# Performance work log

Hardware: AMD Instinct MI355X
Metric: run time of the kernel (lower is better)

The kernel has to match this reference:

```python
import jax, jax.numpy as jnp
import numpy as np

B, DIM, H, W = 8, 128, 112, 112
WSZ, K = 7, 9
D4 = DIM // 4


def setup_inputs() -> dict:
    key = jax.random.key(0)
    ks = jax.random.split(key, 8)
    w = lambda k, shape: jax.random.normal(k, shape, jnp.float32) * 0.05
    return {
        'x_in': jax.random.normal(ks[0], (B, DIM, H, W), jnp.float32),
        'f_w': w(ks[1], (D4, DIM)), 'f_b': jnp.zeros((D4,), jnp.float32),
        'f_gn_w': jnp.ones((D4,), jnp.float32), 'f_gn_b': jnp.zeros((D4,), jnp.float32),
        'p_w': w(ks[2], (DIM, D4)), 'p_b': jnp.zeros((DIM,), jnp.float32),
        'p_gn_w': jnp.ones((DIM,), jnp.float32), 'p_gn_b': jnp.zeros((DIM,), jnp.float32),
        'r_w': w(ks[3], (DIM, DIM)), 'r_b': jnp.zeros((DIM,), jnp.float32),
        'r_gn_w': jnp.ones((DIM,), jnp.float32), 'r_gn_b': jnp.zeros((DIM,), jnp.float32),
        'e1_w': w(ks[4], (D4, 2 * D4)), 'e1_b': jnp.zeros((D4,), jnp.float32),
        'e2_w': w(ks[5], (1, D4)), 'e2_b': jnp.zeros((1,), jnp.float32),
        'gamma': jnp.ones((1,), jnp.float32), 'beta': jnp.zeros((1,), jnp.float32),
    }


def conv1x1(x, w, b):
    # 1x1 conv == channel matmul. x: (B,C,H,W), w: (O,C)
    return jnp.einsum('bchw,oc->bohw', x, w) + b[None, :, None, None]


def gn1(x, w, b, eps=1e-5):
    # GroupNorm(1, C): normalize over (C,H,W) per sample
    mu = x.mean(axis=(1, 2, 3), keepdims=True)
    var = x.var(axis=(1, 2, 3), keepdims=True)
    xn = (x - mu) * jax.lax.rsqrt(var + eps)
    return xn * w[None, :, None, None] + b[None, :, None, None]


def reference(x_in, f_w, f_b, f_gn_w, f_gn_b, p_w, p_b, p_gn_w, p_gn_b,
              r_w, r_b, r_gn_w, r_gn_b, e1_w, e1_b, e2_w, e2_b, gamma, beta):
    b, c, h, w_ = x_in.shape
    wg = hg = WSZ
    pw, ph = h // wg, w_ // hg  # per-window spatial dims (16,16)

    residual = gn1(conv1x1(x_in, r_w, r_b), r_gn_w, r_gn_b)

    # 'b c (Wg w) (Hg h) -> (b Wg Hg) c w h'
    x = x_in.reshape(b, c, wg, pw, hg, ph).transpose(0, 2, 4, 1, 3, 5)
    x = x.reshape(b * wg * hg, c, pw, ph)

    f = gn1(conv1x1(x, f_w, f_b), f_gn_w, f_gn_b)  # (Bp, D4, pw, ph)
    bp, c4, hp, wp = f.shape
    n = hp * wp

    xf = f.reshape(bp, c4, n).transpose(0, 2, 1)  # (Bp, N, C4) nodes

    gy, gx = jnp.meshgrid(jnp.arange(hp), jnp.arange(wp), indexing='ij')
    grid = jnp.stack([gy, gx], axis=-1).astype(jnp.float32).reshape(n, 2)
    grid = (grid - grid.mean(0)) / (grid.std(0, ddof=1) + 1e-5)  # torch std is unbiased

    xa = jnp.concatenate([xf, jnp.broadcast_to(grid, (bp, n, 2))], axis=-1)
    xn = xa / jnp.maximum(jnp.linalg.norm(xa, axis=-1, keepdims=True), 1e-8)
    sim = jnp.einsum('bnd,bmd->bnm', xn, xn)  # (Bp, N, N) cosine sim
    sim = jnp.where(jnp.eye(n, dtype=bool), -jnp.inf, sim)
    _, topk_idx = jax.lax.top_k(sim, K)  # (Bp, N, K)

    # gather neighbor messages; scatter_add back to row == sum over K (rows are dense)
    msg = jax.vmap(lambda a, i: a[i])(xf, topk_idx)          # (Bp, N, K, C4)
    src = jnp.broadcast_to(xf[:, :, None, :], msg.shape)      # (Bp, N, K, C4)
    ef = jnp.concatenate([src, msg], axis=-1)                 # (Bp, N, K, 2*C4)
    h1 = jax.nn.silu(ef @ e1_w.T + e1_b)
    wgt = jax.nn.sigmoid(h1 @ e2_w.T + e2_b)[..., 0]          # (Bp, N, K)
    out = (msg * wgt[..., None]).sum(axis=2)                  # (Bp, N, C4)

    out = out * gamma + xf * beta
    out = out.reshape(bp, hp, wp, c4).transpose(0, 3, 1, 2)   # (Bp, C4, hp, wp)

    # '(b Wg Hg) c w h -> b c (Wg w) (Hg h)'
    out = out.reshape(b, wg, hg, c4, hp, wp).transpose(0, 3, 1, 4, 2, 5)
    out = out.reshape(b, c4, h, w_)

    out = gn1(conv1x1(out, p_w, p_b), p_gn_w, p_gn_b) + residual
    return out
```

## Files before the change

kernel.cpp:

```cpp
#include <hip/hip_runtime.h>
#include <hip/hip_fp16.h>
#include <math.h>

#define CIN 128
#define C4  32
#define HW  12544
#define KNB 9
#define NWIN 392

__device__ inline double wave_sum(double v) {
#pragma unroll
    for (int off = 32; off; off >>= 1) v += __shfl_down(v, off);
    return v;
}

#define TOP9_INSERT(sv, mi, tv, ti)                                  \
    {                                                                \
        _Pragma("unroll")                                            \
        for (int j = KNB - 1; j >= 1; --j) {                         \
            bool cj  = (sv) > tv[j];                                 \
            bool cjm = (sv) > tv[j - 1];                             \
            tv[j] = cj ? (cjm ? tv[j - 1] : (sv)) : tv[j];           \
            ti[j] = cj ? (cjm ? ti[j - 1] : (mi)) : ti[j];           \
        }                                                            \
        bool c0 = (sv) > tv[0];                                      \
        tv[0] = c0 ? (sv) : tv[0];                                   \
        ti[0] = c0 ? (mi) : ti[0];                                   \
    }

__global__ __launch_bounds__(256) void prep_kernel(
    const float* __restrict__ f_w, const float* __restrict__ r_w,
    const float* __restrict__ p_w,
    double* __restrict__ fw64t, float* __restrict__ rwt_t, float* __restrict__ pwt_t)
{
    const int i = blockIdx.x * 256 + threadIdx.x;
    if (i < 4096)  fw64t[(i & 127) * 32 + (i >> 7)]  = (double)f_w[i];
    if (i < 16384) rwt_t[(i & 127) * 128 + (i >> 7)] = r_w[i];
    if (i < 4096)  pwt_t[(i & 31) * 128 + (i >> 5)]  = p_w[i];
}

__global__ __launch_bounds__(512, 6) void fconv_rstats_kernel(
    const float* __restrict__ x_in,
    const double* __restrict__ fw64t, const float* __restrict__ f_b,
    const float* __restrict__ f_gn_w, const float* __restrict__ f_gn_b,
    const float* __restrict__ rwt_t, const float* __restrict__ r_b,
    float* __restrict__ xfws, double* __restrict__ invnws,
    double* __restrict__ stats)
{
    __shared__ __align__(16) char smem[34944];
    double* vbuf = (double*)smem;
    double* red  = (double*)(smem + 34816);
    const int t = threadIdx.x;

    if (blockIdx.x < NWIN) {
        const int win = blockIdx.x;
        const int b = win / 49, wg = (win / 7) % 7, hg = win % 7;
        const int n = t & 255, s = t >> 8;
        const int py = n >> 4, px = n & 15;
        const int rs = __builtin_amdgcn_readfirstlane(s);

        const float* xb = x_in + (size_t)b * CIN * HW + (size_t)(wg * 16 + py) * 112 + (hg * 16 + px);
        const double* wB = fw64t + 16 * rs;
        double acc[16];
#pragma unroll
        for (int j = 0; j < 16; ++j) acc[j] = 0.0;
#pragma unroll 2
        for (int c = 0; c < CIN; ++c) {
            double xv = (double)xb[(size_t)c * HW];
            const double* wr = wB + c * 32;
#pragma unroll
            for (int j = 0; j < 16; ++j) acc[j] = fma(wr[j], xv, acc[j]);
        }
        double s1 = 0.0, s2 = 0.0;
#pragma unroll
        for (int j = 0; j < 16; ++j) {
            double v = acc[j] + (double)f_b[16 * rs + j];
            acc[j] = v; s1 += v; s2 += v * v;
        }
        s1 = wave_sum(s1); s2 = wave_sum(s2);
        {
            int w = t >> 6;
            if ((t & 63) == 0) { red[w] = s1; red[8 + w] = s2; }
        }
        __syncthreads();
        double rs1 = 0.0, rs2 = 0.0;
#pragma unroll
        for (int w = 0; w < 8; ++w) { rs1 += red[w]; rs2 += red[8 + w]; }
        const double mu   = rs1 * (1.0 / 8192.0);
        const double var  = rs2 * (1.0 / 8192.0) - mu * mu;
        const double rstd = 1.0 / sqrt(var + 1e-5);

        float myv[16];
#pragma unroll
        for (int j = 0; j < 16; ++j) {
            int c = 16 * rs + j;
            myv[j] = (float)((acc[j] - mu) * rstd * (double)f_gn_w[c] + (double)f_gn_b[c]);
        }
        float* xrow = xfws + (size_t)(win * 256 + n) * 36;
#pragma unroll
        for (int q4 = 0; q4 < 4; ++q4) {
            float4 f = { myv[4 * q4], myv[4 * q4 + 1], myv[4 * q4 + 2], myv[4 * q4 + 3] };
            ((float4*)(xrow + 16 * rs))[q4] = f;
        }
        const double ginv = 1.0 / (sqrt(5440.0 / 255.0) + 1e-5);
        const float gyf = (float)(((double)py - 7.5) * ginv);
        const float gxf = (float)(((double)px - 7.5) * ginv);
        if (s == 0) {
            float4 g4 = { gyf, gxf, 0.f, 0.f };
            ((float4*)(xrow + 32))[0] = g4;
        }
        if (s == 1) {
#pragma unroll
            for (int j = 0; j < 16; ++j) vbuf[n * 17 + j] = (double)myv[j];
        }
        __syncthreads();
        if (s == 0) {
            double nrm = 0.0;
#pragma unroll
            for (int j = 0; j < 16; ++j) { double x = (double)myv[j]; nrm += x * x; }
#pragma unroll
            for (int j = 0; j < 16; ++j) { double x = vbuf[n * 17 + j]; nrm += x * x; }
            double xg = (double)gyf; nrm += xg * xg;
            double xh = (double)gxf; nrm += xh * xh;
            invnws[win * 256 + n] = 1.0 / fmax(sqrt(nrm), 1e-8);
        }
    } else {
        const int idx = blockIdx.x - NWIN;
        const int b = idx / 98, rem = idx % 98;
        const int oc = rem / 49, pg = rem % 49;
        const int sh = t >> 8, n = t & 255;
        const int rsh = __builtin_amdgcn_readfirstlane(sh);
        const float* wR = rwt_t + oc * 64 + rsh * 32;
        const float* xb = x_in + (size_t)b * CIN * HW + pg * 256 + n;
        float acc[32];
#pragma unroll
        for (int o = 0; o < 32; ++o) acc[o] = r_b[oc * 64 + rsh * 32 + o];
#pragma unroll 2
        for (int c = 0; c < CIN; ++c) {
            float xv = xb[(size_t)c * HW];
            const float* wr = wR + c * 128;
#pragma unroll
            for (int o = 0; o < 32; ++o) acc[o] = fmaf(wr[o], xv, acc[o]);
        }
        double s1 = 0.0, s2 = 0.0;
#pragma unroll
        for (int o = 0; o < 32; ++o) { double v = (double)acc[o]; s1 += v; s2 += v * v; }
        s1 = wave_sum(s1); s2 = wave_sum(s2);
        {
            int w = t >> 6;
            if ((t & 63) == 0) { red[w] = s1; red[8 + w] = s2; }
        }
        __syncthreads();
        if (t == 0) {
            double a = 0.0, c = 0.0;
#pragma unroll
            for (int w = 0; w < 8; ++w) { a += red[w]; c += red[8 + w]; }
            atomicAdd(&stats[b * 4 + 0], a);
            atomicAdd(&stats[b * 4 + 1], c);
        }
    }
}

__global__ __launch_bounds__(256, 4) void sim_hm_kernel(
    const float* __restrict__ xfws, const double* __restrict__ invnws,
    const float* __restrict__ e1_w,
    float* __restrict__ pval, unsigned char* __restrict__ pidx,
    __half* __restrict__ hmws)
{
    const int bid = blockIdx.x;
    if (bid < 4 * NWIN) {
        const int win = bid >> 2, m0 = (bid & 3) << 6;
        const int n = threadIdx.x;

        double xad[34];
        {
            const float4* own = (const float4*)(xfws + (size_t)(win * 256 + n) * 36);
#pragma unroll
            for (int q = 0; q < 8; ++q) {
                float4 f = own[q];
                xad[q * 4 + 0] = (double)f.x; xad[q * 4 + 1] = (double)f.y;
                xad[q * 4 + 2] = (double)f.z; xad[q * 4 + 3] = (double)f.w;
            }
            float4 g = own[8];
            xad[32] = (double)g.x; xad[33] = (double)g.y;
        }
        const double inv_self = invnws[(size_t)win * 256 + n];
        const float*  xmb  = xfws + (size_t)(win * 256 + m0) * 36;
        const double* invb = invnws + (size_t)win * 256 + m0;

        float tv[KNB]; int ti[KNB];
#pragma unroll
        for (int k = 0; k < KNB; ++k) { tv[k] = -INFINITY; ti[k] = 0; }
#pragma unroll 2
        for (int mm = 0; mm < 64; ++mm) {
            const float* xm = xmb + mm * 36;
            double d0 = 0.0, d1 = 0.0, d2 = 0.0, d3 = 0.0;
#pragma unroll
            for (int q = 0; q < 8; ++q) {
                d0 = fma((double)xm[4 * q + 0], xad[4 * q + 0], d0);
                d1 = fma((double)xm[4 * q + 1], xad[4 * q + 1], d1);
                d2 = fma((double)xm[4 * q + 2], xad[4 * q + 2], d2);
                d3 = fma((double)xm[4 * q + 3], xad[4 * q + 3], d3);
            }
            d0 = fma((double)xm[32], xad[32], d0);
            d1 = fma((double)xm[33], xad[33], d1);
            double d = (d0 + d1) + (d2 + d3);
            float sv = (float)(d * (inv_self * invb[mm]));
            sv = (m0 + mm == n) ? -INFINITY : sv;
            TOP9_INSERT(sv, m0 + mm, tv, ti);
        }
        const size_t base = ((size_t)bid * 256 + n) * 9;
#pragma unroll
        for (int k = 0; k < KNB; ++k) { pval[base + k] = tv[k]; pidx[base + k] = (unsigned char)ti[k]; }
    } else {
        const int idxm = bid - 4 * NWIN;
        const int win = idxm >> 1, half = idxm & 1;
        const int t = threadIdx.x;
        const int n = t & 127;
        const int jh = __builtin_amdgcn_readfirstlane(t >> 7);
        const int gn = half * 128 + n;
        const float4* xr4 = (const float4*)(xfws + (size_t)(win * 256 + gn) * 36);
        float xr[32];
#pragma unroll
        for (int q = 0; q < 8; ++q) {
            float4 f = xr4[q];
            xr[4 * q + 0] = f.x; xr[4 * q + 1] = f.y;
            xr[4 * q + 2] = f.z; xr[4 * q + 3] = f.w;
        }
        __align__(16) __half hv[16];
#pragma unroll
        for (int jj = 0; jj < 16; ++jj) {
            const float* w = e1_w + (16 * jh + jj) * 64 + 32;
            float a = 0.f;
#pragma unroll
            for (int c = 0; c < C4; ++c) a = fmaf(w[c], xr[c], a);
            hv[jj] = __float2half_rn(a);
        }
        float4* dst = (float4*)(hmws + (size_t)(win * 256 + gn) * 32 + 16 * jh);
        dst[0] = ((const float4*)hv)[0];
        dst[1] = ((const float4*)hv)[1];
    }
}

__global__ __launch_bounds__(512, 6) void merge_mlp_kernel(
    const float* __restrict__ xfws, const __half* __restrict__ hmws,
    const float* __restrict__ pval, const unsigned char* __restrict__ pidx,
    const float* __restrict__ e1_w, const float* __restrict__ e1_b,
    const float* __restrict__ e2_w, const float* __restrict__ e2_b,
    const float* __restrict__ gamma, const float* __restrict__ beta,
    float* __restrict__ gnn)
{
    __shared__ __align__(16) char smem[50432];
    __half2* xf2 = (__half2*)smem;
    __half2* hm2 = (__half2*)(smem + 17408);
    __half2* hs2 = (__half2*)(smem + 34816);
    short*   Ti  = (short*)(smem + 43520);
    float*   Wt  = (float*)(smem + 45824);

    const int bid = blockIdx.x;
    const int win = bid >> 1, half = bid & 1;
    const int b = win / 49, wg = (win / 7) % 7, hg = win % 7;
    const int t = threadIdx.x;
    const int nl = t & 127, s = t >> 7;
    const int gn = half * 128 + nl;
    const int rs = __builtin_amdgcn_readfirstlane(s);

    {
        const int r = t >> 1, hh = t & 1;
        const float4* sx = (const float4*)(xfws + (size_t)win * 9216 + r * 36 + hh * 16);
#pragma unroll
        for (int q = 0; q < 4; ++q) {
            float4 f = sx[q];
            xf2[r * 17 + hh * 8 + 2 * q]     = __floats2half2_rn(f.x, f.y);
            xf2[r * 17 + hh * 8 + 2 * q + 1] = __floats2half2_rn(f.z, f.w);
        }
        const uint4* sh = (const uint4*)(hmws + (size_t)win * 8192 + r * 32 + hh * 16);
        uint4 u0 = sh[0], u1 = sh[1];
        unsigned int* d = (unsigned int*)(hm2 + r * 17 + hh * 8);
        d[0] = u0.x; d[1] = u0.y; d[2] = u0.z; d[3] = u0.w;
        d[4] = u1.x; d[5] = u1.y; d[6] = u1.z; d[7] = u1.w;
    }
    __syncthreads();

    {
        float xr[C4];
#pragma unroll
        for (int q = 0; q < 16; ++q) {
            float2 f = __half22float2(xf2[gn * 17 + q]);
            xr[2 * q] = f.x; xr[2 * q + 1] = f.y;
        }
        float hsv[8];
#pragma unroll
        for (int jj = 0; jj < 8; ++jj) {
            const int j = 8 * rs + jj;
            const float* w = e1_w + j * 64;
            float h0 = e1_b[j], h1 = 0.f;
#pragma unroll
            for (int c = 0; c < C4; c += 2) {
                h0 = fmaf(w[c], xr[c], h0);
                h1 = fmaf(w[c + 1], xr[c + 1], h1);
            }
            hsv[jj] = h0 + h1;
        }
#pragma unroll
        for (int u = 0; u < 4; ++u)
            hs2[nl * 17 + 4 * rs + u] = __floats2half2_rn(hsv[2 * u], hsv[2 * u + 1]);
    }
    if (s == 0) {
        float tv[KNB]; int ti[KNB];
#pragma unroll
        for (int k = 0; k < KNB; ++k) { tv[k] = -INFINITY; ti[k] = 0; }
        for (int qd = 0; qd < 4; ++qd) {
            const size_t base = ((size_t)(win * 4 + qd) * 256 + gn) * 9;
#pragma unroll
            for (int k = 0; k < KNB; ++k) {
                float sv = pval[base + k];
                int   mi = (int)pidx[base + k];
                TOP9_INSERT(sv, mi, tv, ti);
            }
        }
#pragma unroll
        for (int k = 0; k < KNB; ++k) Ti[nl * 9 + k] = (short)ti[k];
    }
    __syncthreads();

    {
        float hsr[C4];
#pragma unroll
        for (int q = 0; q < 16; ++q) {
            float2 f = __half22float2(hs2[nl * 17 + q]);
            hsr[2 * q] = f.x; hsr[2 * q + 1] = f.y;
        }
        const float e2b = e2_b[0];
        for (int k = s; k < KNB; k += 4) {
            const int m = (int)Ti[nl * 9 + k];
            float a2 = 0.f;
#pragma unroll
            for (int jp = 0; jp < 16; ++jp) {
                float2 hv = __half22float2(hm2[m * 17 + jp]);
                float h0 = hsr[2 * jp] + hv.x;
                float h1 = hsr[2 * jp + 1] + hv.y;
                float sg0 = 1.f / (1.f + __expf(-h0));
                a2 = fmaf(e2_w[2 * jp], h0 * sg0, a2);
                float sg1 = 1.f / (1.f + __expf(-h1));
                a2 = fmaf(e2_w[2 * jp + 1], h1 * sg1, a2);
            }
            Wt[nl * 9 + k] = 1.f / (1.f + __expf(-(a2 + e2b)));
        }
    }
    __syncthreads();

    {
        short tis[KNB]; float wks[KNB];
#pragma unroll
        for (int k = 0; k < KNB; ++k) { tis[k] = Ti[nl * 9 + k]; wks[k] = Wt[nl * 9 + k]; }
        const float g = gamma[0], be = beta[0];
        const int py = gn >> 4, px = gn & 15;
        float* gp = gnn + (size_t)b * C4 * HW + (size_t)(wg * 16 + py) * 112 + (hg * 16 + px);
        float xo[8];
#pragma unroll
        for (int q = 0; q < 4; ++q) {
            float2 f = __half22float2(xf2[gn * 17 + 4 * rs + q]);
            xo[2 * q] = f.x; xo[2 * q + 1] = f.y;
        }
        float o[8];
#pragma unroll
        for (int cc = 0; cc < 8; ++cc) o[cc] = 0.f;
#pragma unroll
        for (int k = 0; k < KNB; ++k) {
            const int mrow = (int)tis[k] * 17 + 4 * rs;
#pragma unroll
            for (int q = 0; q < 4; ++q) {
                float2 mv = __half22float2(xf2[mrow + q]);
                o[2 * q]     = fmaf(wks[k], mv.x, o[2 * q]);
                o[2 * q + 1] = fmaf(wks[k], mv.y, o[2 * q + 1]);
            }
        }
#pragma unroll
        for (int cc = 0; cc < 8; ++cc) {
            float gl = fmaf(g, o[cc], be * xo[cc]);
            gp[(size_t)(8 * rs + cc) * HW] = gl;
        }
    }
}

__global__ __launch_bounds__(256, 8) void pstats_kernel(
    const float* __restrict__ gnn, const float* __restrict__ p_w,
    const float* __restrict__ p_b, double* __restrict__ stats)
{
    __shared__ double red[16];
    const int idx = blockIdx.x;
    const int b = idx / 98, pg = idx % 98;
    const int t = threadIdx.x;
    const int pix = pg * 128 + (t & 127);
    const int oh = __builtin_amdgcn_readfirstlane(t >> 7);

    const float* gb = gnn + (size_t)b * C4 * HW + pix;
    float g[C4];
#pragma unroll
    for (int c = 0; c < C4; ++c) g[c] = gb[(size_t)c * HW];

    double s1 = 0.0, s2 = 0.0;
    const float* pwb = p_w + (size_t)oh * 64 * C4;
#pragma unroll 4
    for (int o = 0; o < 64; ++o) {
        const float* w = pwb + o * C4;
        float y = p_b[oh * 64 + o];
#pragma unroll
        for (int c = 0; c < C4; ++c) y = fmaf(w[c], g[c], y);
        s1 += (double)y; s2 += (double)y * (double)y;
    }
    s1 = wave_sum(s1); s2 = wave_sum(s2);
    {
        int w = t >> 6;
        if ((t & 63) == 0) { red[w] = s1; red[8 + w] = s2; }
    }
    __syncthreads();
    if (t == 0) {
        double a = 0.0, c = 0.0;
#pragma unroll
        for (int w = 0; w < 4; ++w) { a += red[w]; c += red[8 + w]; }
        atomicAdd(&stats[b * 4 + 2], a);
        atomicAdd(&stats[b * 4 + 3], c);
    }
}

__global__ __launch_bounds__(256) void final_kernel(
    const float* __restrict__ x_in, const float* __restrict__ gnn,
    const float* __restrict__ rwt_t, const float* __restrict__ r_b,
    const float* __restrict__ r_gn_w, const float* __restrict__ r_gn_b,
    const float* __restrict__ pwt_t, const float* __restrict__ p_b,
    const float* __restrict__ p_gn_w, const float* __restrict__ p_gn_b,
    const double* __restrict__ stats,
    float* __restrict__ out)
{
    const int idx = blockIdx.x;
    const int b = idx / 196, rem = idx % 196;
    const int ocq = rem / 49, pg = rem % 49;
    const int t = threadIdx.x;

    const double NN = (double)CIN * HW;
    const double mu_r = stats[b * 4 + 0] / NN;
    const float  rs_r = (float)(1.0 / sqrt(stats[b * 4 + 1] / NN - mu_r * mu_r + 1e-5));
    const double mu_p = stats[b * 4 + 2] / NN;
    const float  rs_p = (float)(1.0 / sqrt(stats[b * 4 + 3] / NN - mu_p * mu_p + 1e-5));
    const float fmur = (float)mu_r, fmup = (float)mu_p;

    const int p = pg * 256 + t;
    const float* xb = x_in + (size_t)b * CIN * HW + p;
    const float* gb = gnn + (size_t)b * C4 * HW + p;
    float* ob = out + (size_t)b * CIN * HW + p;

    float xg[C4];
#pragma unroll
    for (int c = 0; c < C4; ++c) xg[c] = gb[(size_t)c * HW];

    float accR[32], accP[32];
#pragma unroll
    for (int o = 0; o < 32; ++o) {
        accR[o] = r_b[ocq * 32 + o];
        accP[o] = p_b[ocq * 32 + o];
    }
#pragma unroll 2
    for (int c = 0; c < CIN; ++c) {
        float xv = xb[(size_t)c * HW];
        const float* w = rwt_t + c * 128 + ocq * 32;
#pragma unroll
        for (int o = 0; o < 32; ++o) accR[o] = fmaf(w[o], xv, accR[o]);
    }
#pragma unroll
    for (int c = 0; c < C4; ++c) {
        const float* w = pwt_t + c * 128 + ocq * 32;
#pragma unroll
        for (int o = 0; o < 32; ++o) accP[o] = fmaf(w[o], xg[c], accP[o]);
    }
#pragma unroll
    for (int o = 0; o < 32; ++o) {
        const int O = ocq * 32 + o;
        float yr = (accR[o] - fmur) * rs_r * r_gn_w[O] + r_gn_b[O];
        float yp = (accP[o] - fmup) * rs_p * p_gn_w[O] + p_gn_b[O];
        ob[(size_t)O * HW] = yp + yr;
    }
}

extern "C" void kernel_launch(void* const* d_in, const int* in_sizes, int n_in,
                              void* d_out, int out_size, void* d_ws, size_t ws_size,
                              hipStream_t stream)
{
    const float* x_in   = (const float*)d_in[0];
    const float* f_w    = (const float*)d_in[1];
    const float* f_b    = (const float*)d_in[2];
    const float* f_gn_w = (const float*)d_in[3];
    const float* f_gn_b = (const float*)d_in[4];
    const float* p_w    = (const float*)d_in[5];
    const float* p_b    = (const float*)d_in[6];
    const float* p_gn_w = (const float*)d_in[7];
    const float* p_gn_b = (const float*)d_in[8];
    const float* r_w    = (const float*)d_in[9];
    const float* r_b    = (const float*)d_in[10];
    const float* r_gn_w = (const float*)d_in[11];
    const float* r_gn_b = (const float*)d_in[12];
    const float* e1_w   = (const float*)d_in[13];
    const float* e1_b   = (const float*)d_in[14];
    const float* e2_w   = (const float*)d_in[15];
    const float* e2_b   = (const float*)d_in[16];
    const float* gamma  = (const float*)d_in[17];
    const float* beta   = (const float*)d_in[18];

    char* wsb = (char*)d_ws;
    float*         gnn    = (float*)        (wsb + 0);
    double*        stats  = (double*)       (wsb + 12845056);
    float*         xfws   = (float*)        (wsb + 12845312);
    double*        invnws = (double*)       (wsb + 27296000);
    float*         pval   = (float*)        (wsb + 28098816);
    unsigned char* pidx   = (unsigned char*)(wsb + 42549504);
    double*        fw64t  = (double*)       (wsb + 46162176);
    float*         rwt_t  = (float*)        (wsb + 46194944);
    float*         pwt_t  = (float*)        (wsb + 46260480);
    __half*        hmws   = (__half*)       (wsb + 46276864);

    hipMemsetAsync(stats, 0, 32 * sizeof(double), stream);
    prep_kernel<<<64, 256, 0, stream>>>(f_w, r_w, p_w, fw64t, rwt_t, pwt_t);
    fconv_rstats_kernel<<<NWIN + 784, 512, 0, stream>>>(
        x_in, fw64t, f_b, f_gn_w, f_gn_b, rwt_t, r_b, xfws, invnws, stats);
    sim_hm_kernel<<<NWIN * 4 + NWIN * 2, 256, 0, stream>>>(
        xfws, invnws, e1_w, pval, pidx, hmws);
    merge_mlp_kernel<<<NWIN * 2, 512, 0, stream>>>(
        xfws, hmws, pval, pidx, e1_w, e1_b, e2_w, e2_b, gamma, beta, gnn);
    pstats_kernel<<<784, 256, 0, stream>>>(gnn, p_w, p_b, stats);
    final_kernel<<<1568, 256, 0, stream>>>(
        x_in, gnn, rwt_t, r_b, r_gn_w, r_gn_b, pwt_t, p_b, p_gn_w, p_gn_b, stats, (float*)d_out);
}
```

Measured before the change: 327.4 us.

## Store node features as fp64 and halve similarity partitions per window

```diff
diff --git a/kernel.cpp b/kernel.cpp
--- a/kernel.cpp
+++ b/kernel.cpp
@@ -44,7 +44,7 @@
     const double* __restrict__ fw64t, const float* __restrict__ f_b,
     const float* __restrict__ f_gn_w, const float* __restrict__ f_gn_b,
     const float* __restrict__ rwt_t, const float* __restrict__ r_b,
-    float* __restrict__ xfws, double* __restrict__ invnws,
+    double* __restrict__ xf64, double* __restrict__ invnws,
     double* __restrict__ stats)
 {
     __shared__ __align__(16) char smem[34944];
@@ -96,18 +96,18 @@
             int c = 16 * rs + j;
             myv[j] = (float)((acc[j] - mu) * rstd * (double)f_gn_w[c] + (double)f_gn_b[c]);
         }
-        float* xrow = xfws + (size_t)(win * 256 + n) * 36;
-#pragma unroll
-        for (int q4 = 0; q4 < 4; ++q4) {
-            float4 f = { myv[4 * q4], myv[4 * q4 + 1], myv[4 * q4 + 2], myv[4 * q4 + 3] };
-            ((float4*)(xrow + 16 * rs))[q4] = f;
+        double* xrow = xf64 + (size_t)(win * 256 + n) * 34;
+#pragma unroll
+        for (int j2 = 0; j2 < 8; ++j2) {
+            double2 d2 = { (double)myv[2 * j2], (double)myv[2 * j2 + 1] };
+            ((double2*)(xrow + 16 * rs))[j2] = d2;
         }
         const double ginv = 1.0 / (sqrt(5440.0 / 255.0) + 1e-5);
         const float gyf = (float)(((double)py - 7.5) * ginv);
         const float gxf = (float)(((double)px - 7.5) * ginv);
         if (s == 0) {
-            float4 g4 = { gyf, gxf, 0.f, 0.f };
-            ((float4*)(xrow + 32))[0] = g4;
+            double2 g2 = { (double)gyf, (double)gxf };
+            ((double2*)(xrow + 32))[0] = g2;
         }
         if (s == 1) {
 #pragma unroll
@@ -162,48 +162,45 @@
 }
 
 __global__ __launch_bounds__(256, 4) void sim_hm_kernel(
-    const float* __restrict__ xfws, const double* __restrict__ invnws,
+    const double* __restrict__ xf64, const double* __restrict__ invnws,
     const float* __restrict__ e1_w,
     float* __restrict__ pval, unsigned char* __restrict__ pidx,
     __half* __restrict__ hmws)
 {
     const int bid = blockIdx.x;
-    if (bid < 4 * NWIN) {
-        const int win = bid >> 2, m0 = (bid & 3) << 6;
+    if (bid < 2 * NWIN) {
+        const int win = bid >> 1, m0 = (bid & 1) << 7;
         const int n = threadIdx.x;
 
         double xad[34];
         {
-            const float4* own = (const float4*)(xfws + (size_t)(win * 256 + n) * 36);
-#pragma unroll
-            for (int q = 0; q < 8; ++q) {
-                float4 f = own[q];
-                xad[q * 4 + 0] = (double)f.x; xad[q * 4 + 1] = (double)f.y;
-                xad[q * 4 + 2] = (double)f.z; xad[q * 4 + 3] = (double)f.w;
+            const double2* own = (const double2*)(xf64 + (size_t)(win * 256 + n) * 34);
+#pragma unroll
+            for (int q = 0; q < 17; ++q) {
+                double2 d = own[q];
+                xad[2 * q] = d.x; xad[2 * q + 1] = d.y;
             }
-            float4 g = own[8];
-            xad[32] = (double)g.x; xad[33] = (double)g.y;
         }
         const double inv_self = invnws[(size_t)win * 256 + n];
-        const float*  xmb  = xfws + (size_t)(win * 256 + m0) * 36;
+        const double* xmb  = xf64 + (size_t)(win * 256 + m0) * 34;
         const double* invb = invnws + (size_t)win * 256 + m0;
 
         float tv[KNB]; int ti[KNB];
 #pragma unroll
         for (int k = 0; k < KNB; ++k) { tv[k] = -INFINITY; ti[k] = 0; }
 #pragma unroll 2
-        for (int mm = 0; mm < 64; ++mm) {
-            const float* xm = xmb + mm * 36;
+        for (int mm = 0; mm < 128; ++mm) {
+            const double* xm = xmb + mm * 34;
             double d0 = 0.0, d1 = 0.0, d2 = 0.0, d3 = 0.0;
 #pragma unroll
             for (int q = 0; q < 8; ++q) {
-                d0 = fma((double)xm[4 * q + 0], xad[4 * q + 0], d0);
-                d1 = fma((double)xm[4 * q + 1], xad[4 * q + 1], d1);
-                d2 = fma((double)xm[4 * q + 2], xad[4 * q + 2], d2);
-                d3 = fma((double)xm[4 * q + 3], xad[4 * q + 3], d3);
+                d0 = fma(xm[4 * q + 0], xad[4 * q + 0], d0);
+                d1 = fma(xm[4 * q + 1], xad[4 * q + 1], d1);
+                d2 = fma(xm[4 * q + 2], xad[4 * q + 2], d2);
+                d3 = fma(xm[4 * q + 3], xad[4 * q + 3], d3);
             }
-            d0 = fma((double)xm[32], xad[32], d0);
-            d1 = fma((double)xm[33], xad[33], d1);
+            d0 = fma(xm[32], xad[32], d0);
+            d1 = fma(xm[33], xad[33], d1);
             double d = (d0 + d1) + (d2 + d3);
             float sv = (float)(d * (inv_self * invb[mm]));
             sv = (m0 + mm == n) ? -INFINITY : sv;
@@ -213,19 +210,18 @@
 #pragma unroll
         for (int k = 0; k < KNB; ++k) { pval[base + k] = tv[k]; pidx[base + k] = (unsigned char)ti[k]; }
     } else {
-        const int idxm = bid - 4 * NWIN;
+        const int idxm = bid - 2 * NWIN;
         const int win = idxm >> 1, half = idxm & 1;
         const int t = threadIdx.x;
         const int n = t & 127;
         const int jh = __builtin_amdgcn_readfirstlane(t >> 7);
         const int gn = half * 128 + n;
-        const float4* xr4 = (const float4*)(xfws + (size_t)(win * 256 + gn) * 36);
+        const double2* xr2 = (const double2*)(xf64 + (size_t)(win * 256 + gn) * 34);
         float xr[32];
 #pragma unroll
-        for (int q = 0; q < 8; ++q) {
-            float4 f = xr4[q];
-            xr[4 * q + 0] = f.x; xr[4 * q + 1] = f.y;
-            xr[4 * q + 2] = f.z; xr[4 * q + 3] = f.w;
+        for (int q = 0; q < 16; ++q) {
+            double2 d = xr2[q];
+            xr[2 * q] = (float)d.x; xr[2 * q + 1] = (float)d.y;
         }
         __align__(16) __half hv[16];
 #pragma unroll
@@ -243,7 +239,7 @@
 }
 
 __global__ __launch_bounds__(512, 6) void merge_mlp_kernel(
-    const float* __restrict__ xfws, const __half* __restrict__ hmws,
+    const double* __restrict__ xf64, const __half* __restrict__ hmws,
     const float* __restrict__ pval, const unsigned char* __restrict__ pidx,
     const float* __restrict__ e1_w, const float* __restrict__ e1_b,
     const float* __restrict__ e2_w, const float* __restrict__ e2_b,
@@ -267,12 +263,12 @@
 
     {
         const int r = t >> 1, hh = t & 1;
-        const float4* sx = (const float4*)(xfws + (size_t)win * 9216 + r * 36 + hh * 16);
+        const double2* sx = (const double2*)(xf64 + (size_t)win * 256 * 34 + r * 34 + hh * 16);
 #pragma unroll
         for (int q = 0; q < 4; ++q) {
-            float4 f = sx[q];
-            xf2[r * 17 + hh * 8 + 2 * q]     = __floats2half2_rn(f.x, f.y);
-            xf2[r * 17 + hh * 8 + 2 * q + 1] = __floats2half2_rn(f.z, f.w);
+            double2 a = sx[2 * q], b2 = sx[2 * q + 1];
+            xf2[r * 17 + hh * 8 + 2 * q]     = __floats2half2_rn((float)a.x, (float)a.y);
+            xf2[r * 17 + hh * 8 + 2 * q + 1] = __floats2half2_rn((float)b2.x, (float)b2.y);
         }
         const uint4* sh = (const uint4*)(hmws + (size_t)win * 8192 + r * 32 + hh * 16);
         uint4 u0 = sh[0], u1 = sh[1];
@@ -310,8 +306,8 @@
         float tv[KNB]; int ti[KNB];
 #pragma unroll
         for (int k = 0; k < KNB; ++k) { tv[k] = -INFINITY; ti[k] = 0; }
-        for (int qd = 0; qd < 4; ++qd) {
-            const size_t base = ((size_t)(win * 4 + qd) * 256 + gn) * 9;
+        for (int qd = 0; qd < 2; ++qd) {
+            const size_t base = ((size_t)(win * 2 + qd) * 256 + gn) * 9;
 #pragma unroll
             for (int k = 0; k < KNB; ++k) {
                 float sv = pval[base + k];
@@ -510,23 +506,23 @@
     char* wsb = (char*)d_ws;
     float*         gnn    = (float*)        (wsb + 0);
     double*        stats  = (double*)       (wsb + 12845056);
-    float*         xfws   = (float*)        (wsb + 12845312);
-    double*        invnws = (double*)       (wsb + 27296000);
-    float*         pval   = (float*)        (wsb + 28098816);
-    unsigned char* pidx   = (unsigned char*)(wsb + 42549504);
-    double*        fw64t  = (double*)       (wsb + 46162176);
-    float*         rwt_t  = (float*)        (wsb + 46194944);
-    float*         pwt_t  = (float*)        (wsb + 46260480);
-    __half*        hmws   = (__half*)       (wsb + 46276864);
+    double*        invnws = (double*)       (wsb + 12845312);
+    float*         pval   = (float*)        (wsb + 13648128);
+    unsigned char* pidx   = (unsigned char*)(wsb + 20873472);
+    double*        fw64t  = (double*)       (wsb + 22679808);
+    float*         rwt_t  = (float*)        (wsb + 22712576);
+    float*         pwt_t  = (float*)        (wsb + 22778112);
+    __half*        hmws   = (__half*)       (wsb + 22794496);
+    double*        xf64   = (double*)       (wsb + 29217024);
 
     hipMemsetAsync(stats, 0, 32 * sizeof(double), stream);
     prep_kernel<<<64, 256, 0, stream>>>(f_w, r_w, p_w, fw64t, rwt_t, pwt_t);
     fconv_rstats_kernel<<<NWIN + 784, 512, 0, stream>>>(
-        x_in, fw64t, f_b, f_gn_w, f_gn_b, rwt_t, r_b, xfws, invnws, stats);
-    sim_hm_kernel<<<NWIN * 4 + NWIN * 2, 256, 0, stream>>>(
-        xfws, invnws, e1_w, pval, pidx, hmws);
+        x_in, fw64t, f_b, f_gn_w, f_gn_b, rwt_t, r_b, xf64, invnws, stats);
+    sim_hm_kernel<<<NWIN * 2 + NWIN * 2, 256, 0, stream>>>(
+        xf64, invnws, e1_w, pval, pidx, hmws);
     merge_mlp_kernel<<<NWIN * 2, 512, 0, stream>>>(
-        xfws, hmws, pval, pidx, e1_w, e1_b, e2_w, e2_b, gamma, beta, gnn);
+        xf64, hmws, pval, pidx, e1_w, e1_b, e2_w, e2_b, gamma, beta, gnn);
     pstats_kernel<<<784, 256, 0, stream>>>(gnn, p_w, p_b, stats);
     final_kernel<<<1568, 256, 0, stream>>>(
         x_in, gnn, rwt_t, r_b, r_gn_w, r_gn_b, pwt_t, p_b, p_gn_w, p_gn_b, stats, (float*)d_out);
```

Result: slower. 338.0 us (+3.3%).

## Screen kNN candidates in fp32, then rescore top-11 in fp64

Applied to the files above, without the earlier changes.

```diff
diff --git a/kernel.cpp b/kernel.cpp
--- a/kernel.cpp
+++ b/kernel.cpp
@@ -6,6 +6,7 @@
 #define C4  32
 #define HW  12544
 #define KNB 9
+#define KSCR 11
 #define NWIN 392
 
 __device__ inline double wave_sum(double v) {
@@ -14,19 +15,19 @@
     return v;
 }
 
-#define TOP9_INSERT(sv, mi, tv, ti)                                  \
-    {                                                                \
-        _Pragma("unroll")                                            \
-        for (int j = KNB - 1; j >= 1; --j) {                         \
-            bool cj  = (sv) > tv[j];                                 \
-            bool cjm = (sv) > tv[j - 1];                             \
-            tv[j] = cj ? (cjm ? tv[j - 1] : (sv)) : tv[j];           \
-            ti[j] = cj ? (cjm ? ti[j - 1] : (mi)) : ti[j];           \
-        }                                                            \
-        bool c0 = (sv) > tv[0];                                      \
-        tv[0] = c0 ? (sv) : tv[0];                                   \
-        ti[0] = c0 ? (mi) : ti[0];                                   \
-    }
+template <int K>
+__device__ inline void topk_insert(float sv, int mi, float* tv, int* ti) {
+#pragma unroll
+    for (int j = K - 1; j >= 1; --j) {
+        bool cj  = sv > tv[j];
+        bool cjm = sv > tv[j - 1];
+        tv[j] = cj ? (cjm ? tv[j - 1] : sv) : tv[j];
+        ti[j] = cj ? (cjm ? ti[j - 1] : mi) : ti[j];
+    }
+    bool c0 = sv > tv[0];
+    tv[0] = c0 ? sv : tv[0];
+    ti[0] = c0 ? mi : ti[0];
+}
 
 __global__ __launch_bounds__(256) void prep_kernel(
     const float* __restrict__ f_w, const float* __restrict__ r_w,
@@ -44,7 +45,7 @@
     const double* __restrict__ fw64t, const float* __restrict__ f_b,
     const float* __restrict__ f_gn_w, const float* __restrict__ f_gn_b,
     const float* __restrict__ rwt_t, const float* __restrict__ r_b,
-    float* __restrict__ xfws, double* __restrict__ invnws,
+    float* __restrict__ xfws, double* __restrict__ invnws, float* __restrict__ invn32,
     double* __restrict__ stats)
 {
     __shared__ __align__(16) char smem[34944];
@@ -122,7 +123,9 @@
             for (int j = 0; j < 16; ++j) { double x = vbuf[n * 17 + j]; nrm += x * x; }
             double xg = (double)gyf; nrm += xg * xg;
             double xh = (double)gxf; nrm += xh * xh;
-            invnws[win * 256 + n] = 1.0 / fmax(sqrt(nrm), 1e-8);
+            double invd = 1.0 / fmax(sqrt(nrm), 1e-8);
+            invnws[win * 256 + n] = invd;
+            invn32[win * 256 + n] = (float)invd;
         }
     } else {
         const int idx = blockIdx.x - NWIN;
@@ -163,7 +166,7 @@
 
 __global__ __launch_bounds__(256, 4) void sim_hm_kernel(
     const float* __restrict__ xfws, const double* __restrict__ invnws,
-    const float* __restrict__ e1_w,
+    const float* __restrict__ invn32, const float* __restrict__ e1_w,
     float* __restrict__ pval, unsigned char* __restrict__ pidx,
     __half* __restrict__ hmws)
 {
@@ -172,46 +175,80 @@
         const int win = bid >> 2, m0 = (bid & 3) << 6;
         const int n = threadIdx.x;
 
-        double xad[34];
+        float xad[34];
         {
             const float4* own = (const float4*)(xfws + (size_t)(win * 256 + n) * 36);
 #pragma unroll
             for (int q = 0; q < 8; ++q) {
                 float4 f = own[q];
-                xad[q * 4 + 0] = (double)f.x; xad[q * 4 + 1] = (double)f.y;
-                xad[q * 4 + 2] = (double)f.z; xad[q * 4 + 3] = (double)f.w;
+                xad[q * 4 + 0] = f.x; xad[q * 4 + 1] = f.y;
+                xad[q * 4 + 2] = f.z; xad[q * 4 + 3] = f.w;
             }
             float4 g = own[8];
-            xad[32] = (double)g.x; xad[33] = (double)g.y;
-        }
-        const double inv_self = invnws[(size_t)win * 256 + n];
-        const float*  xmb  = xfws + (size_t)(win * 256 + m0) * 36;
-        const double* invb = invnws + (size_t)win * 256 + m0;
-
-        float tv[KNB]; int ti[KNB];
-#pragma unroll
-        for (int k = 0; k < KNB; ++k) { tv[k] = -INFINITY; ti[k] = 0; }
+            xad[32] = g.x; xad[33] = g.y;
+        }
+        const float invs = invn32[(size_t)win * 256 + n];
+        const float* xmb   = xfws + (size_t)(win * 256 + m0) * 36;
+        const float* invb  = invn32 + (size_t)win * 256 + m0;
+
+        float tv[KSCR]; int ti[KSCR];
+#pragma unroll
+        for (int k = 0; k < KSCR; ++k) { tv[k] = -INFINITY; ti[k] = 0; }
 #pragma unroll 2
         for (int mm = 0; mm < 64; ++mm) {
             const float* xm = xmb + mm * 36;
+            float f0 = 0.f, f1 = 0.f, f2 = 0.f, f3 = 0.f;
+#pragma unroll
+            for (int q = 0; q < 8; ++q) {
+                f0 = fmaf(xm[4 * q + 0], xad[4 * q + 0], f0);
+                f1 = fmaf(xm[4 * q + 1], xad[4 * q + 1], f1);
+                f2 = fmaf(xm[4 * q + 2], xad[4 * q + 2], f2);
+                f3 = fmaf(xm[4 * q + 3], xad[4 * q + 3], f3);
+            }
+            f0 = fmaf(xm[32], xad[32], f0);
+            f1 = fmaf(xm[33], xad[33], f1);
+            float sv = ((f0 + f1) + (f2 + f3)) * (invs * invb[mm]);
+            sv = (m0 + mm == n) ? -INFINITY : sv;
+            topk_insert<KSCR>(sv, m0 + mm, tv, ti);
+        }
+
+#pragma unroll
+        for (int p = 0; p < KSCR - 1; ++p)
+#pragma unroll
+            for (int q = 0; q < KSCR - 1 - p; ++q) {
+                int a = ti[q], bb = ti[q + 1];
+                bool sw = a > bb;
+                ti[q] = sw ? bb : a; ti[q + 1] = sw ? a : bb;
+            }
+
+        double xad64[34];
+#pragma unroll
+        for (int c = 0; c < 34; ++c) xad64[c] = (double)xad[c];
+        const double inv_self = invnws[(size_t)win * 256 + n];
+        float tv9[KNB]; int ti9[KNB];
+#pragma unroll
+        for (int k = 0; k < KNB; ++k) { tv9[k] = -INFINITY; ti9[k] = 0; }
+#pragma unroll
+        for (int k = 0; k < KSCR; ++k) {
+            const int mi = ti[k];
+            const float* xm = xfws + (size_t)(win * 256 + mi) * 36;
             double d0 = 0.0, d1 = 0.0, d2 = 0.0, d3 = 0.0;
 #pragma unroll
             for (int q = 0; q < 8; ++q) {
-                d0 = fma((double)xm[4 * q + 0], xad[4 * q + 0], d0);
-                d1 = fma((double)xm[4 * q + 1], xad[4 * q + 1], d1);
-                d2 = fma((double)xm[4 * q + 2], xad[4 * q + 2], d2);
-                d3 = fma((double)xm[4 * q + 3], xad[4 * q + 3], d3);
-            }
-            d0 = fma((double)xm[32], xad[32], d0);
-            d1 = fma((double)xm[33], xad[33], d1);
+                d0 = fma((double)xm[4 * q + 0], xad64[4 * q + 0], d0);
+                d1 = fma((double)xm[4 * q + 1], xad64[4 * q + 1], d1);
+                d2 = fma((double)xm[4 * q + 2], xad64[4 * q + 2], d2);
+                d3 = fma((double)xm[4 * q + 3], xad64[4 * q + 3], d3);
+            }
+            d0 = fma((double)xm[32], xad64[32], d0);
+            d1 = fma((double)xm[33], xad64[33], d1);
             double d = (d0 + d1) + (d2 + d3);
-            float sv = (float)(d * (inv_self * invb[mm]));
-            sv = (m0 + mm == n) ? -INFINITY : sv;
-            TOP9_INSERT(sv, m0 + mm, tv, ti);
+            float sv = (float)(d * (inv_self * invnws[(size_t)win * 256 + mi]));
+            topk_insert<KNB>(sv, mi, tv9, ti9);
         }
         const size_t base = ((size_t)bid * 256 + n) * 9;
 #pragma unroll
-        for (int k = 0; k < KNB; ++k) { pval[base + k] = tv[k]; pidx[base + k] = (unsigned char)ti[k]; }
+        for (int k = 0; k < KNB; ++k) { pval[base + k] = tv9[k]; pidx[base + k] = (unsigned char)ti9[k]; }
     } else {
         const int idxm = bid - 4 * NWIN;
         const int win = idxm >> 1, half = idxm & 1;
@@ -316,7 +353,7 @@
             for (int k = 0; k < KNB; ++k) {
                 float sv = pval[base + k];
                 int   mi = (int)pidx[base + k];
-                TOP9_INSERT(sv, mi, tv, ti);
+                topk_insert<KNB>(sv, mi, tv, ti);
             }
         }
 #pragma unroll
@@ -518,13 +555,14 @@
     float*         rwt_t  = (float*)        (wsb + 46194944);
     float*         pwt_t  = (float*)        (wsb + 46260480);
     __half*        hmws   = (__half*)       (wsb + 46276864);
+    float*         invn32 = (float*)        (wsb + 52699392);
 
     hipMemsetAsync(stats, 0, 32 * sizeof(double), stream);
     prep_kernel<<<64, 256, 0, stream>>>(f_w, r_w, p_w, fw64t, rwt_t, pwt_t);
     fconv_rstats_kernel<<<NWIN + 784, 512, 0, stream>>>(
-        x_in, fw64t, f_b, f_gn_w, f_gn_b, rwt_t, r_b, xfws, invnws, stats);
+        x_in, fw64t, f_b, f_gn_w, f_gn_b, rwt_t, r_b, xfws, invnws, invn32, stats);
     sim_hm_kernel<<<NWIN * 4 + NWIN * 2, 256, 0, stream>>>(
-        xfws, invnws, e1_w, pval, pidx, hmws);
+        xfws, invnws, invn32, e1_w, pval, pidx, hmws);
     merge_mlp_kernel<<<NWIN * 2, 512, 0, stream>>>(
         xfws, hmws, pval, pidx, e1_w, e1_b, e2_w, e2_b, gamma, beta, gnn);
     pstats_kernel<<<784, 256, 0, stream>>>(gnn, p_w, p_b, stats);
```

Result: slower. 386.2 us (+18.0%).

## Fold weight prep into fconv and move residual stats into sim kernel

Applied to the files above, without the earlier changes.

```diff
diff --git a/kernel.cpp b/kernel.cpp
--- a/kernel.cpp
+++ b/kernel.cpp
@@ -14,10 +14,10 @@
     return v;
 }
 
-#define TOP9_INSERT(sv, mi, tv, ti)                                  \
+#define TOPK_INSERT(K, sv, mi, tv, ti)                               \
     {                                                                \
         _Pragma("unroll")                                            \
-        for (int j = KNB - 1; j >= 1; --j) {                         \
+        for (int j = (K) - 1; j >= 1; --j) {                         \
             bool cj  = (sv) > tv[j];                                 \
             bool cjm = (sv) > tv[j - 1];                             \
             tv[j] = cj ? (cjm ? tv[j - 1] : (sv)) : tv[j];           \
@@ -28,48 +28,50 @@
         ti[0] = c0 ? (mi) : ti[0];                                   \
     }
 
-__global__ __launch_bounds__(256) void prep_kernel(
-    const float* __restrict__ f_w, const float* __restrict__ r_w,
-    const float* __restrict__ p_w,
-    double* __restrict__ fw64t, float* __restrict__ rwt_t, float* __restrict__ pwt_t)
-{
-    const int i = blockIdx.x * 256 + threadIdx.x;
-    if (i < 4096)  fw64t[(i & 127) * 32 + (i >> 7)]  = (double)f_w[i];
-    if (i < 16384) rwt_t[(i & 127) * 128 + (i >> 7)] = r_w[i];
-    if (i < 4096)  pwt_t[(i & 31) * 128 + (i >> 5)]  = p_w[i];
-}
-
-__global__ __launch_bounds__(512, 6) void fconv_rstats_kernel(
+__global__ __launch_bounds__(512, 2) void fconv_prep_kernel(
     const float* __restrict__ x_in,
-    const double* __restrict__ fw64t, const float* __restrict__ f_b,
+    const float* __restrict__ f_w, const float* __restrict__ f_b,
     const float* __restrict__ f_gn_w, const float* __restrict__ f_gn_b,
-    const float* __restrict__ rwt_t, const float* __restrict__ r_b,
+    const float* __restrict__ r_w, const float* __restrict__ p_w,
     float* __restrict__ xfws, double* __restrict__ invnws,
-    double* __restrict__ stats)
+    float* __restrict__ rwt_t, float* __restrict__ pwt_t)
 {
     __shared__ __align__(16) char smem[34944];
-    double* vbuf = (double*)smem;
-    double* red  = (double*)(smem + 34816);
     const int t = threadIdx.x;
 
     if (blockIdx.x < NWIN) {
+        double* wbufd = (double*)smem;
+        double* vbuf  = (double*)smem;
+        double* red   = (double*)(smem + 34816);
         const int win = blockIdx.x;
         const int b = win / 49, wg = (win / 7) % 7, hg = win % 7;
         const int n = t & 255, s = t >> 8;
         const int py = n >> 4, px = n & 15;
         const int rs = __builtin_amdgcn_readfirstlane(s);
 
+        for (int i = t; i < C4 * CIN; i += 512) {
+            int o = i >> 7, c = i & 127;
+            wbufd[(c >> 1) * 64 + o * 2 + (c & 1)] = (double)f_w[i];
+        }
+        __syncthreads();
+
         const float* xb = x_in + (size_t)b * CIN * HW + (size_t)(wg * 16 + py) * 112 + (hg * 16 + px);
-        const double* wB = fw64t + 16 * rs;
         double acc[16];
 #pragma unroll
         for (int j = 0; j < 16; ++j) acc[j] = 0.0;
-#pragma unroll 2
-        for (int c = 0; c < CIN; ++c) {
-            double xv = (double)xb[(size_t)c * HW];
-            const double* wr = wB + c * 32;
-#pragma unroll
-            for (int j = 0; j < 16; ++j) acc[j] = fma(wr[j], xv, acc[j]);
+        {
+            const double2* wrow = (const double2*)wbufd + 16 * rs;
+            for (int c2 = 0; c2 < 64; ++c2) {
+                double xv0 = (double)xb[(size_t)(2 * c2) * HW];
+                double xv1 = (double)xb[(size_t)(2 * c2 + 1) * HW];
+                const double2* wr = wrow + c2 * 32;
+#pragma unroll
+                for (int j = 0; j < 16; ++j) {
+                    double2 w2 = wr[j];
+                    acc[j] = fma(w2.x, xv0, acc[j]);
+                    acc[j] = fma(w2.y, xv1, acc[j]);
+                }
+            }
         }
         double s1 = 0.0, s2 = 0.0;
 #pragma unroll
@@ -125,48 +127,21 @@
             invnws[win * 256 + n] = 1.0 / fmax(sqrt(nrm), 1e-8);
         }
     } else {
-        const int idx = blockIdx.x - NWIN;
-        const int b = idx / 98, rem = idx % 98;
-        const int oc = rem / 49, pg = rem % 49;
-        const int sh = t >> 8, n = t & 255;
-        const int rsh = __builtin_amdgcn_readfirstlane(sh);
-        const float* wR = rwt_t + oc * 64 + rsh * 32;
-        const float* xb = x_in + (size_t)b * CIN * HW + pg * 256 + n;
-        float acc[32];
-#pragma unroll
-        for (int o = 0; o < 32; ++o) acc[o] = r_b[oc * 64 + rsh * 32 + o];
-#pragma unroll 2
-        for (int c = 0; c < CIN; ++c) {
-            float xv = xb[(size_t)c * HW];
-            const float* wr = wR + c * 128;
-#pragma unroll
-            for (int o = 0; o < 32; ++o) acc[o] = fmaf(wr[o], xv, acc[o]);
-        }
-        double s1 = 0.0, s2 = 0.0;
-#pragma unroll
-        for (int o = 0; o < 32; ++o) { double v = (double)acc[o]; s1 += v; s2 += v * v; }
-        s1 = wave_sum(s1); s2 = wave_sum(s2);
-        {
-            int w = t >> 6;
-            if ((t & 63) == 0) { red[w] = s1; red[8 + w] = s2; }
-        }
-        __syncthreads();
-        if (t == 0) {
-            double a = 0.0, c = 0.0;
-#pragma unroll
-            for (int w = 0; w < 8; ++w) { a += red[w]; c += red[8 + w]; }
-            atomicAdd(&stats[b * 4 + 0], a);
-            atomicAdd(&stats[b * 4 + 1], c);
-        }
-    }
-}
-
-__global__ __launch_bounds__(256, 4) void sim_hm_kernel(
+        const int i = (blockIdx.x - NWIN) * 512 + t;
+        if (i < 16384) rwt_t[(i & 127) * 128 + (i >> 7)] = r_w[i];
+        if (i < 4096)  pwt_t[(i & 31) * 128 + (i >> 5)]  = p_w[i];
+    }
+}
+
+__global__ __launch_bounds__(256, 4) void sim_hm_rstats_kernel(
+    const float* __restrict__ x_in,
     const float* __restrict__ xfws, const double* __restrict__ invnws,
     const float* __restrict__ e1_w,
+    const float* __restrict__ rwt_t, const float* __restrict__ r_b,
     float* __restrict__ pval, unsigned char* __restrict__ pidx,
-    __half* __restrict__ hmws)
+    __half* __restrict__ hmws, double* __restrict__ stats)
 {
+    __shared__ double red[16];
     const int bid = blockIdx.x;
     if (bid < 4 * NWIN) {
         const int win = bid >> 2, m0 = (bid & 3) << 6;
@@ -207,12 +182,12 @@
             double d = (d0 + d1) + (d2 + d3);
             float sv = (float)(d * (inv_self * invb[mm]));
             sv = (m0 + mm == n) ? -INFINITY : sv;
-            TOP9_INSERT(sv, m0 + mm, tv, ti);
+            TOPK_INSERT(KNB, sv, m0 + mm, tv, ti);
         }
         const size_t base = ((size_t)bid * 256 + n) * 9;
 #pragma unroll
         for (int k = 0; k < KNB; ++k) { pval[base + k] = tv[k]; pidx[base + k] = (unsigned char)ti[k]; }
-    } else {
+    } else if (bid < 6 * NWIN) {
         const int idxm = bid - 4 * NWIN;
         const int win = idxm >> 1, half = idxm & 1;
         const int t = threadIdx.x;
@@ -239,6 +214,38 @@
         float4* dst = (float4*)(hmws + (size_t)(win * 256 + gn) * 32 + 16 * jh);
         dst[0] = ((const float4*)hv)[0];
         dst[1] = ((const float4*)hv)[1];
+    } else {
+        const int idx = bid - 6 * NWIN;
+        const int b = idx / 196, rem = idx % 196;
+        const int oc = rem / 49, pg = rem % 49;
+        const int t = threadIdx.x;
+        const float* xb = x_in + (size_t)b * CIN * HW + pg * 256 + t;
+        float acc[32];
+#pragma unroll
+        for (int o = 0; o < 32; ++o) acc[o] = r_b[oc * 32 + o];
+#pragma unroll 2
+        for (int c = 0; c < CIN; ++c) {
+            float xv = xb[(size_t)c * HW];
+            const float* wr = rwt_t + c * 128 + oc * 32;
+#pragma unroll
+            for (int o = 0; o < 32; ++o) acc[o] = fmaf(wr[o], xv, acc[o]);
+        }
+        double s1 = 0.0, s2 = 0.0;
+#pragma unroll
+        for (int o = 0; o < 32; ++o) { double v = (double)acc[o]; s1 += v; s2 += v * v; }
+        s1 = wave_sum(s1); s2 = wave_sum(s2);
+        {
+            int w = t >> 6;
+            if ((t & 63) == 0) { red[w] = s1; red[8 + w] = s2; }
+        }
+        __syncthreads();
+        if (t == 0) {
+            double a = 0.0, c = 0.0;
+#pragma unroll
+            for (int w = 0; w < 4; ++w) { a += red[w]; c += red[8 + w]; }
+            atomicAdd(&stats[b * 4 + 0], a);
+            atomicAdd(&stats[b * 4 + 1], c);
+        }
     }
 }
 
@@ -316,7 +323,7 @@
             for (int k = 0; k < KNB; ++k) {
                 float sv = pval[base + k];
                 int   mi = (int)pidx[base + k];
-                TOP9_INSERT(sv, mi, tv, ti);
+                TOPK_INSERT(KNB, sv, mi, tv, ti);
             }
         }
 #pragma unroll
@@ -514,17 +521,15 @@
     double*        invnws = (double*)       (wsb + 27296000);
     float*         pval   = (float*)        (wsb + 28098816);
     unsigned char* pidx   = (unsigned char*)(wsb + 42549504);
-    double*        fw64t  = (double*)       (wsb + 46162176);
-    float*         rwt_t  = (float*)        (wsb + 46194944);
-    float*         pwt_t  = (float*)        (wsb + 46260480);
-    __half*        hmws   = (__half*)       (wsb + 46276864);
+    float*         rwt_t  = (float*)        (wsb + 46162176);
+    float*         pwt_t  = (float*)        (wsb + 46227712);
+    __half*        hmws   = (__half*)       (wsb + 46244096);
 
     hipMemsetAsync(stats, 0, 32 * sizeof(double), stream);
-    prep_kernel<<<64, 256, 0, stream>>>(f_w, r_w, p_w, fw64t, rwt_t, pwt_t);
-    fconv_rstats_kernel<<<NWIN + 784, 512, 0, stream>>>(
-        x_in, fw64t, f_b, f_gn_w, f_gn_b, rwt_t, r_b, xfws, invnws, stats);
-    sim_hm_kernel<<<NWIN * 4 + NWIN * 2, 256, 0, stream>>>(
-        xfws, invnws, e1_w, pval, pidx, hmws);
+    fconv_prep_kernel<<<NWIN + 32, 512, 0, stream>>>(
+        x_in, f_w, f_b, f_gn_w, f_gn_b, r_w, p_w, xfws, invnws, rwt_t, pwt_t);
+    sim_hm_rstats_kernel<<<NWIN * 4 + NWIN * 2 + 1568, 256, 0, stream>>>(
+        x_in, xfws, invnws, e1_w, rwt_t, r_b, pval, pidx, hmws, stats);
     merge_mlp_kernel<<<NWIN * 2, 512, 0, stream>>>(
         xfws, hmws, pval, pidx, e1_w, e1_b, e2_w, e2_b, gamma, beta, gnn);
     pstats_kernel<<<784, 256, 0, stream>>>(gnn, p_w, p_b, stats);
```

New measurement: 347.2 us. 1.06x slower.
